# Kernel optimization log

Measured on AMD Instinct MI355X. Metric: run time of the kernel, lower is better.

The kernel has to match this reference:

```python
import jax, jax.numpy as jnp
import numpy as np

RADIUS = 51        # radius=50 in __init__ gets +1 because it is even
WEIGHT = 0.5       # forward default
THRESHOLD = 10.0   # forward default


def gaussian_kernel_2d(ksize):
    # cv2.getGaussianKernel(ksize, 0): sigma = 0.3*((ksize-1)*0.5 - 1) + 0.8
    sigma = 0.3 * ((ksize - 1) * 0.5 - 1.0) + 0.8
    x = np.arange(ksize, dtype=np.float64) - (ksize - 1) * 0.5
    k1 = np.exp(-(x * x) / (2.0 * sigma * sigma))
    k1 /= k1.sum()
    return (k1[:, None] * k1[None, :]).astype(np.float32)  # outer product, sums to 1


def _filter2d(img, kernel):
    # basicsr filter2D: reflect-pad then depthwise (per-channel) valid 2D conv
    c = img.shape[1]
    p = kernel.shape[-1] // 2
    imgp = jnp.pad(img, ((0, 0), (0, 0), (p, p), (p, p)), mode='reflect')
    k = jnp.broadcast_to(kernel[None, None], (c, 1, kernel.shape[0], kernel.shape[1]))
    return jax.lax.conv_general_dilated(
        imgp, k, window_strides=(1, 1), padding='VALID',
        dimension_numbers=('NCHW', 'OIHW', 'NCHW'), feature_group_count=c)


def setup_inputs() -> dict:
    key = jax.random.key(0)
    img = jax.random.uniform(key, (2, 3, 1080, 1920), dtype=jnp.float32)  # [B,C,H,W] in [0,1]
    kernel = jnp.asarray(gaussian_kernel_2d(RADIUS))  # [51,51] Gaussian buffer
    return {"img": img, "kernel": kernel}


def reference(img, kernel):
    blur = _filter2d(img, kernel)
    residual = img - blur
    mask = (jnp.abs(residual) * 255.0 > THRESHOLD).astype(img.dtype)
    soft_mask = _filter2d(mask, kernel)
    sharp = jnp.clip(img + WEIGHT * residual, 0.0, 1.0)
    return soft_mask * sharp + (1.0 - soft_mask) * img
```

## Files before the change

### kernel.cpp

```cpp
#include <hip/hip_runtime.h>


#define W 1920
#define H 1080
#define NP 6
#define PLANE (H * W)
#define TOT (NP * PLANE)
#define R 25
#define KS 51
#define TV 9
#define NXT 15
#define NYT 15
#define WU_TOTAL (NXT * NYT * NP)
#define WU_PER_XCD ((WU_TOTAL + 7) / 8)
#define NROWS (H * NP)
#define NI (NROWS * 116)
#define NBI ((NI + 255) / 256)
#define NB (NROWS * 4)
#define NBB ((NB + 255) / 256)

__device__ __forceinline__ int reflect_idx(int i, int n) {
    if (i < 0) i = -i;
    if (i >= n) i = 2 * n - 2 - i;
    return i;
}
__device__ __forceinline__ float bf2f(unsigned short u) {
    return __uint_as_float(((unsigned int)u) << 16);
}
__device__ __forceinline__ unsigned short f2bf(float f) {
    unsigned int x = __float_as_uint(f);
    return (unsigned short)((x + 0x7FFFu + ((x >> 16) & 1u)) >> 16);
}
__device__ __forceinline__ float maskf(float f) {
    return (fabsf(f) * 255.f > 10.f) ? 1.f : 0.f;
}

__global__ void compute_k1(const float* __restrict__ k2d, float* __restrict__ k1) {
    int t = threadIdx.x;
    if (t < KS) {
        float s = 0.f;
        for (int j = 0; j < KS; ++j) s += k2d[t * KS + j];
        k1[t] = s;
    }
}

#define CONTRIB(P, VV)                                                   \
    {                                                                    \
        const int _p = (P);                                              \
        if (_p >= 7 && _p <= 72) {                                       \
            const int _olo = (_p - 57 > 0) ? _p - 57 : 0;                \
            const int _ohi = (_p - 7 < 15) ? _p - 7 : 15;                \
            _Pragma("unroll") for (int o = _olo; o <= _ohi; ++o)         \
                acc[o] += k1g[_p - 7 - o] * (VV);                        \
        }                                                                \
    }

template <bool MASK>
__global__ void hblur16(const void* __restrict__ inv, unsigned short* __restrict__ out,
                        const float* __restrict__ k1g) {
    const int b = blockIdx.x;
    float acc[16];
#pragma unroll
    for (int o = 0; o < 16; ++o) acc[o] = 0.f;
    int row, c0;
    if (b < NBI) {
        const int t = b * 256 + threadIdx.x;
        if (t >= NI) return;
        row = t / 116;
        c0 = (2 + (t - row * 116)) * 16;
        if constexpr (!MASK) {
            const float* rin = (const float*)inv + (size_t)row * W;
#pragma unroll
            for (int i = 0; i < 20; ++i) {
                float4 v = *(const float4*)(rin + c0 - 32 + 4 * i);
                CONTRIB(4 * i + 0, v.x);
                CONTRIB(4 * i + 1, v.y);
                CONTRIB(4 * i + 2, v.z);
                CONTRIB(4 * i + 3, v.w);
            }
        } else {
            const unsigned short* rin = (const unsigned short*)inv + (size_t)row * W;
#pragma unroll
            for (int i = 0; i < 10; ++i) {
                uint4 u = *(const uint4*)(rin + c0 - 32 + 8 * i);
#pragma unroll
                for (int h = 0; h < 4; ++h) {
                    const unsigned int c = (h == 0) ? u.x : (h == 1) ? u.y : (h == 2) ? u.z : u.w;
                    const float flo = __uint_as_float(c << 16);
                    const float fhi = __uint_as_float(c & 0xffff0000u);
                    CONTRIB(8 * i + 2 * h + 0, maskf(flo));
                    CONTRIB(8 * i + 2 * h + 1, maskf(fhi));
                }
            }
        }
    } else {
        const int t = (b - NBI) * 256 + threadIdx.x;
        if (t >= NB) return;
        row = t >> 2;
        const int q = t & 3;
        c0 = ((q < 2) ? q : q + 116) * 16;
        if constexpr (!MASK) {
            const float* rin = (const float*)inv + (size_t)row * W;
#pragma unroll
            for (int i = 7; i <= 72; ++i) {
                float vv = rin[reflect_idx(c0 - 32 + i, W)];
                CONTRIB(i, vv);
            }
        } else {
            const unsigned short* rin = (const unsigned short*)inv + (size_t)row * W;
#pragma unroll
            for (int i = 7; i <= 72; ++i) {
                float vv = maskf(bf2f(rin[reflect_idx(c0 - 32 + i, W)]));
                CONTRIB(i, vv);
            }
        }
    }
    uint4 o0, o1;
    o0.x = (unsigned int)f2bf(acc[0]) | ((unsigned int)f2bf(acc[1]) << 16);
    o0.y = (unsigned int)f2bf(acc[2]) | ((unsigned int)f2bf(acc[3]) << 16);
    o0.z = (unsigned int)f2bf(acc[4]) | ((unsigned int)f2bf(acc[5]) << 16);
    o0.w = (unsigned int)f2bf(acc[6]) | ((unsigned int)f2bf(acc[7]) << 16);
    o1.x = (unsigned int)f2bf(acc[8]) | ((unsigned int)f2bf(acc[9]) << 16);
    o1.y = (unsigned int)f2bf(acc[10]) | ((unsigned int)f2bf(acc[11]) << 16);
    o1.z = (unsigned int)f2bf(acc[12]) | ((unsigned int)f2bf(acc[13]) << 16);
    o1.w = (unsigned int)f2bf(acc[14]) | ((unsigned int)f2bf(acc[15]) << 16);
    unsigned short* op = out + (size_t)row * W + c0;
    *(uint4*)op = o0;
    *(uint4*)(op + 8) = o1;
}

__device__ __forceinline__ bool decode_wu(int lin, int& p, int& yt, int& xt) {
    int c = lin & 7, j = lin >> 3;
    int wu = c * WU_PER_XCD + j;
    if (wu >= WU_TOTAL) return false;
    p = wu / (NXT * NYT);
    int rem = wu - p * (NXT * NYT);
    yt = rem / NXT;
    xt = rem - yt * NXT;
    return true;
}

__device__ __forceinline__ void vconv9(const unsigned short* __restrict__ Ap, int x4, int y0,
                                       const float* __restrict__ k1g, float4 acc[TV]) {
#pragma unroll
    for (int j = 0; j < TV; ++j) acc[j] = make_float4(0.f, 0.f, 0.f, 0.f);
    if (y0 >= R && y0 + TV - 1 + R < H) {
        const unsigned short* p = Ap + (size_t)(y0 - R) * W + x4;
#pragma unroll
        for (int u = 0; u < TV + 2 * R; ++u) {
            ushort4 s = *(const ushort4*)p;
            p += W;
            float4 v = make_float4(bf2f(s.x), bf2f(s.y), bf2f(s.z), bf2f(s.w));
            const int jlo = (u - 2 * R > 0) ? u - 2 * R : 0;
            const int jhi = (u < TV - 1) ? u : TV - 1;
#pragma unroll
            for (int j = jlo; j <= jhi; ++j) {
                const float k = k1g[u - j];
                acc[j].x += k * v.x; acc[j].y += k * v.y;
                acc[j].z += k * v.z; acc[j].w += k * v.w;
            }
        }
    } else {
#pragma unroll
        for (int u = 0; u < TV + 2 * R; ++u) {
            int yy = reflect_idx(y0 - R + u, H);
            ushort4 s = *(const ushort4*)(Ap + (size_t)yy * W + x4);
            float4 v = make_float4(bf2f(s.x), bf2f(s.y), bf2f(s.z), bf2f(s.w));
            const int jlo = (u - 2 * R > 0) ? u - 2 * R : 0;
            const int jhi = (u < TV - 1) ? u : TV - 1;
#pragma unroll
            for (int j = jlo; j <= jhi; ++j) {
                const float k = k1g[u - j];
                acc[j].x += k * v.x; acc[j].y += k * v.y;
                acc[j].z += k * v.z; acc[j].w += k * v.w;
            }
        }
    }
}

__global__ void vblur_r(const unsigned short* __restrict__ A, const float* __restrict__ img,
                        const float* __restrict__ k1g, unsigned short* __restrict__ rbuf) {
    int p, yt, xt;
    if (!decode_wu(blockIdx.x, p, yt, xt)) return;
    const int tx = threadIdx.x & 31, ty = threadIdx.x >> 5;
    const int x4 = xt * 128 + tx * 4;
    const int y0 = yt * 72 + ty * TV;
    float4 acc[TV];
    vconv9(A + (size_t)p * PLANE, x4, y0, k1g, acc);
#pragma unroll
    for (int j = 0; j < TV; ++j) {
        size_t idx = (size_t)p * PLANE + (size_t)(y0 + j) * W + x4;
        float4 iv = *(const float4*)&img[idx];
        ushort4 rr;
        rr.x = f2bf(iv.x - acc[j].x);
        rr.y = f2bf(iv.y - acc[j].y);
        rr.z = f2bf(iv.z - acc[j].z);
        rr.w = f2bf(iv.w - acc[j].w);
        *(ushort4*)&rbuf[idx] = rr;
    }
}

__global__ void vblur_blend(const unsigned short* __restrict__ Bh, const float* __restrict__ img,
                            const unsigned short* __restrict__ rbuf,
                            const float* __restrict__ k1g, float* __restrict__ out) {
    int p, yt, xt;
    if (!decode_wu(blockIdx.x, p, yt, xt)) return;
    const int tx = threadIdx.x & 31, ty = threadIdx.x >> 5;
    const int x4 = xt * 128 + tx * 4;
    const int y0 = yt * 72 + ty * TV;
    float4 acc[TV];
    vconv9(Bh + (size_t)p * PLANE, x4, y0, k1g, acc);
#pragma unroll
    for (int j = 0; j < TV; ++j) {
        size_t idx = (size_t)p * PLANE + (size_t)(y0 + j) * W + x4;
        float4 iv = *(const float4*)&img[idx];
        ushort4 ru = *(const ushort4*)&rbuf[idx];
        float dx = fminf(fmaxf(iv.x + 0.5f * bf2f(ru.x), 0.f), 1.f) - iv.x;
        float dy = fminf(fmaxf(iv.y + 0.5f * bf2f(ru.y), 0.f), 1.f) - iv.y;
        float dz = fminf(fmaxf(iv.z + 0.5f * bf2f(ru.z), 0.f), 1.f) - iv.z;
        float dw = fminf(fmaxf(iv.w + 0.5f * bf2f(ru.w), 0.f), 1.f) - iv.w;
        float4 o;
        o.x = iv.x + acc[j].x * dx;
        o.y = iv.y + acc[j].y * dy;
        o.z = iv.z + acc[j].z * dz;
        o.w = iv.w + acc[j].w * dw;
        *(float4*)&out[idx] = o;
    }
}

extern "C" void kernel_launch(void* const* d_in, const int* in_sizes, int n_in,
                              void* d_out, int out_size, void* d_ws, size_t ws_size,
                              hipStream_t stream) {
    const float* img = (const float*)d_in[0];
    const float* k2d = (const float*)d_in[1];
    float* out = (float*)d_out;

    unsigned short* AB = (unsigned short*)d_ws;
    unsigned short* rbuf = AB + TOT;
    float* k1 = (float*)(rbuf + TOT);

    const int gridHB = NBI + NBB;
    const int gridVB = 8 * WU_PER_XCD;

    hipLaunchKernelGGL(compute_k1, dim3(1), dim3(64), 0, stream, k2d, k1);
    hipLaunchKernelGGL((hblur16<false>), dim3(gridHB), dim3(256), 0, stream, (const void*)img, AB, k1);
    hipLaunchKernelGGL(vblur_r, dim3(gridVB), dim3(256), 0, stream, AB, img, k1, rbuf);
    hipLaunchKernelGGL((hblur16<true>), dim3(gridHB), dim3(256), 0, stream, (const void*)rbuf, AB, k1);
    hipLaunchKernelGGL(vblur_blend, dim3(gridVB), dim3(256), 0, stream, AB, img, rbuf, k1, out);
}
```

Before: 228.4 us.

## Stage vertical blur input tile in LDS via direct global-to-LDS loads

The two vertical-blur kernels become one templated kernel that first copies the 122-row by 128-column bf16 input window into shared memory using global_load_lds. It then runs the 59-tap vertical convolution from LDS instead of issuing overlapping global loads per thread. This removes the redundant halo reads, since each 9-row thread strip previously re-fetched 50 neighbouring rows from cache or global memory, and it folds the reflect handling into the staging step. In exchange it adds an LDS footprint of 32 KB per block, a block barrier, and launch bounds that may limit occupancy or registers.

```diff
diff --git a/kernel.cpp b/kernel.cpp
--- a/kernel.cpp
+++ b/kernel.cpp
@@ -18,6 +18,7 @@
 #define NBI ((NI + 255) / 256)
 #define NB (NROWS * 4)
 #define NBB ((NB + 255) / 256)
+#define TROWS 128
 
 __device__ __forceinline__ int reflect_idx(int i, int n) {
     if (i < 0) i = -i;
@@ -140,91 +141,78 @@
     return true;
 }
 
-__device__ __forceinline__ void vconv9(const unsigned short* __restrict__ Ap, int x4, int y0,
-                                       const float* __restrict__ k1g, float4 acc[TV]) {
-#pragma unroll
-    for (int j = 0; j < TV; ++j) acc[j] = make_float4(0.f, 0.f, 0.f, 0.f);
-    if (y0 >= R && y0 + TV - 1 + R < H) {
-        const unsigned short* p = Ap + (size_t)(y0 - R) * W + x4;
-#pragma unroll
-        for (int u = 0; u < TV + 2 * R; ++u) {
-            ushort4 s = *(const ushort4*)p;
-            p += W;
-            float4 v = make_float4(bf2f(s.x), bf2f(s.y), bf2f(s.z), bf2f(s.w));
-            const int jlo = (u - 2 * R > 0) ? u - 2 * R : 0;
-            const int jhi = (u < TV - 1) ? u : TV - 1;
-#pragma unroll
-            for (int j = jlo; j <= jhi; ++j) {
-                const float k = k1g[u - j];
-                acc[j].x += k * v.x; acc[j].y += k * v.y;
-                acc[j].z += k * v.z; acc[j].w += k * v.w;
-            }
-        }
-    } else {
-#pragma unroll
-        for (int u = 0; u < TV + 2 * R; ++u) {
-            int yy = reflect_idx(y0 - R + u, H);
-            ushort4 s = *(const ushort4*)(Ap + (size_t)yy * W + x4);
-            float4 v = make_float4(bf2f(s.x), bf2f(s.y), bf2f(s.z), bf2f(s.w));
-            const int jlo = (u - 2 * R > 0) ? u - 2 * R : 0;
-            const int jhi = (u < TV - 1) ? u : TV - 1;
-#pragma unroll
-            for (int j = jlo; j <= jhi; ++j) {
-                const float k = k1g[u - j];
-                acc[j].x += k * v.x; acc[j].y += k * v.y;
-                acc[j].z += k * v.z; acc[j].w += k * v.w;
-            }
-        }
-    }
-}
-
-__global__ void vblur_r(const unsigned short* __restrict__ A, const float* __restrict__ img,
-                        const float* __restrict__ k1g, unsigned short* __restrict__ rbuf) {
+template <bool BLEND>
+__global__ void __launch_bounds__(256, 4)
+vblur_lds(const unsigned short* __restrict__ A, const float* __restrict__ img,
+          unsigned short* __restrict__ rbuf, const float* __restrict__ k1g,
+          float* __restrict__ outf) {
+    __shared__ unsigned short tile[TROWS * 128];
     int p, yt, xt;
     if (!decode_wu(blockIdx.x, p, yt, xt)) return;
     const int tx = threadIdx.x & 31, ty = threadIdx.x >> 5;
     const int x4 = xt * 128 + tx * 4;
-    const int y0 = yt * 72 + ty * TV;
+    const int y0 = yt * 72;
+    const unsigned short* Ap = A + (size_t)p * PLANE + (size_t)xt * 128;
+
+    const int wave = threadIdx.x >> 6;
+    const int lane = threadIdx.x & 63;
+    const int lrow = lane >> 4;
+    const int lcol = (lane & 15) * 8;
+#pragma unroll
+    for (int i = 0; i < 8; ++i) {
+        const int rbase = wave * 32 + i * 4;
+        if (rbase > 121) continue;
+        const int yy = reflect_idx(y0 - R + rbase + lrow, H);
+        const unsigned short* src = Ap + (size_t)yy * W + lcol;
+        __builtin_amdgcn_global_load_lds(
+            (const __attribute__((address_space(1))) unsigned int*)(const void*)src,
+            (__attribute__((address_space(3))) unsigned int*)(void*)&tile[rbase * 128],
+            16, 0, 0);
+    }
+    __syncthreads();
+
     float4 acc[TV];
-    vconv9(A + (size_t)p * PLANE, x4, y0, k1g, acc);
+#pragma unroll
+    for (int j = 0; j < TV; ++j) acc[j] = make_float4(0.f, 0.f, 0.f, 0.f);
+    const unsigned short* trow = &tile[(ty * TV) * 128 + tx * 4];
+#pragma unroll
+    for (int u = 0; u < TV + 2 * R; ++u) {
+        ushort4 s = *(const ushort4*)(trow + u * 128);
+        float4 v = make_float4(bf2f(s.x), bf2f(s.y), bf2f(s.z), bf2f(s.w));
+        const int jlo = (u - 2 * R > 0) ? u - 2 * R : 0;
+        const int jhi = (u < TV - 1) ? u : TV - 1;
+#pragma unroll
+        for (int j = jlo; j <= jhi; ++j) {
+            const float k = k1g[u - j];
+            acc[j].x += k * v.x; acc[j].y += k * v.y;
+            acc[j].z += k * v.z; acc[j].w += k * v.w;
+        }
+    }
+
 #pragma unroll
     for (int j = 0; j < TV; ++j) {
-        size_t idx = (size_t)p * PLANE + (size_t)(y0 + j) * W + x4;
+        size_t idx = (size_t)p * PLANE + (size_t)(y0 + ty * TV + j) * W + x4;
         float4 iv = *(const float4*)&img[idx];
-        ushort4 rr;
-        rr.x = f2bf(iv.x - acc[j].x);
-        rr.y = f2bf(iv.y - acc[j].y);
-        rr.z = f2bf(iv.z - acc[j].z);
-        rr.w = f2bf(iv.w - acc[j].w);
-        *(ushort4*)&rbuf[idx] = rr;
-    }
-}
-
-__global__ void vblur_blend(const unsigned short* __restrict__ Bh, const float* __restrict__ img,
-                            const unsigned short* __restrict__ rbuf,
-                            const float* __restrict__ k1g, float* __restrict__ out) {
-    int p, yt, xt;
-    if (!decode_wu(blockIdx.x, p, yt, xt)) return;
-    const int tx = threadIdx.x & 31, ty = threadIdx.x >> 5;
-    const int x4 = xt * 128 + tx * 4;
-    const int y0 = yt * 72 + ty * TV;
-    float4 acc[TV];
-    vconv9(Bh + (size_t)p * PLANE, x4, y0, k1g, acc);
-#pragma unroll
-    for (int j = 0; j < TV; ++j) {
-        size_t idx = (size_t)p * PLANE + (size_t)(y0 + j) * W + x4;
-        float4 iv = *(const float4*)&img[idx];
-        ushort4 ru = *(const ushort4*)&rbuf[idx];
-        float dx = fminf(fmaxf(iv.x + 0.5f * bf2f(ru.x), 0.f), 1.f) - iv.x;
-        float dy = fminf(fmaxf(iv.y + 0.5f * bf2f(ru.y), 0.f), 1.f) - iv.y;
-        float dz = fminf(fmaxf(iv.z + 0.5f * bf2f(ru.z), 0.f), 1.f) - iv.z;
-        float dw = fminf(fmaxf(iv.w + 0.5f * bf2f(ru.w), 0.f), 1.f) - iv.w;
-        float4 o;
-        o.x = iv.x + acc[j].x * dx;
-        o.y = iv.y + acc[j].y * dy;
-        o.z = iv.z + acc[j].z * dz;
-        o.w = iv.w + acc[j].w * dw;
-        *(float4*)&out[idx] = o;
+        if constexpr (!BLEND) {
+            ushort4 rr;
+            rr.x = f2bf(iv.x - acc[j].x);
+            rr.y = f2bf(iv.y - acc[j].y);
+            rr.z = f2bf(iv.z - acc[j].z);
+            rr.w = f2bf(iv.w - acc[j].w);
+            *(ushort4*)&rbuf[idx] = rr;
+        } else {
+            ushort4 ru = *(const ushort4*)&rbuf[idx];
+            float dx = fminf(fmaxf(iv.x + 0.5f * bf2f(ru.x), 0.f), 1.f) - iv.x;
+            float dy = fminf(fmaxf(iv.y + 0.5f * bf2f(ru.y), 0.f), 1.f) - iv.y;
+            float dz = fminf(fmaxf(iv.z + 0.5f * bf2f(ru.z), 0.f), 1.f) - iv.z;
+            float dw = fminf(fmaxf(iv.w + 0.5f * bf2f(ru.w), 0.f), 1.f) - iv.w;
+            float4 o;
+            o.x = iv.x + acc[j].x * dx;
+            o.y = iv.y + acc[j].y * dy;
+            o.z = iv.z + acc[j].z * dz;
+            o.w = iv.w + acc[j].w * dw;
+            *(float4*)&outf[idx] = o;
+        }
     }
 }
 
@@ -244,7 +232,7 @@
 
     hipLaunchKernelGGL(compute_k1, dim3(1), dim3(64), 0, stream, k2d, k1);
     hipLaunchKernelGGL((hblur16<false>), dim3(gridHB), dim3(256), 0, stream, (const void*)img, AB, k1);
-    hipLaunchKernelGGL(vblur_r, dim3(gridVB), dim3(256), 0, stream, AB, img, k1, rbuf);
+    hipLaunchKernelGGL((vblur_lds<false>), dim3(gridVB), dim3(256), 0, stream, AB, img, rbuf, k1, out);
     hipLaunchKernelGGL((hblur16<true>), dim3(gridHB), dim3(256), 0, stream, (const void*)rbuf, AB, k1);
-    hipLaunchKernelGGL(vblur_blend, dim3(gridVB), dim3(256), 0, stream, AB, img, rbuf, k1, out);
-}
+    hipLaunchKernelGGL((vblur_lds<true>), dim3(gridVB), dim3(256), 0, stream, AB, img, rbuf, k1, out);
+}
```

New measurement: 340.0 us. 1.49x slower.
